# Performance work log

Measured on AMD Instinct MI355X. Metric: run time of the kernel, lower is better.

The kernel has to match this reference:

```python
import jax, jax.numpy as jnp
import numpy as np

H, W = 192, 640
MAX_ITERS = 200
EPS = 1e-8


def setup_inputs() -> dict:
    key = jax.random.key(0)
    k1, k2 = jax.random.split(key)
    B = 16
    ptcloud = jax.random.normal(k1, (B, 3, H * W), dtype=jnp.float32)
    # KITTI-like intrinsics; cy = 96 so the ground prior starts at row 96.
    Kmat = jnp.tile(
        jnp.array([[721.5, 0.0, 320.0], [0.0, 721.5, 96.0], [0.0, 0.0, 1.0]],
                  dtype=jnp.float32)[None], (B, 1, 1))
    ys = 96
    xs, xe = W * 3 // 8, W * 5 // 8
    n_prior = (H - ys) * (xe - xs)  # 15360
    sample_idx = jax.random.randint(k2, (MAX_ITERS, 3), 0, n_prior, dtype=jnp.int32)
    return {"ptcloud": ptcloud, "K": Kmat, "sample_idx": sample_idx}


def _median_low(x):
    """torch.median semantics (lower middle element), x: (B, N) -> (B, 1)."""
    n = x.shape[1]
    s = jnp.sort(x, axis=1)
    m = (n - 1) // 2
    return s[:, m:m + 1]


def _mad_threshold(y):
    med = _median_low(y)                       # (B, 1)
    return _median_low(jnp.abs(med - y))       # (B, 1)


def _ransac_plane(prior, sample_idx, thr):
    """prior: (B, N, 3), sample_idx: (I, 3), thr: (B, 1) -> plane (B, 4)."""
    samples = prior[:, sample_idx]             # (B, I, 3, 3)
    p1, p2, p3 = samples[:, :, 0], samples[:, :, 1], samples[:, :, 2]
    n = jnp.cross(p2 - p1, p3 - p1)            # (B, I, 3)
    n = n / (jnp.linalg.norm(n, axis=-1, keepdims=True) + EPS)
    d = -jnp.sum(n * p1, axis=-1)              # (B, I)
    # point-plane distances for all prior points: (B, I, N)
    dist = jnp.abs(jnp.einsum('bnc,bic->bin', prior, n) + d[:, :, None])
    counts = jnp.sum(dist <= thr[:, :, None], axis=-1)  # (B, I)
    best = jnp.argmax(counts, axis=1)                    # (B,)
    plane = jnp.concatenate([n, d[..., None]], axis=-1)  # (B, I, 4)
    return jnp.take_along_axis(plane, best[:, None, None], axis=1)[:, 0]


def reference(ptcloud, K, sample_idx):
    B = ptcloud.shape[0]
    # ground prior region (static slice; K is concrete at trace time here)
    ys = int(K[:, 1, 2].mean())
    xs, xe = W * 3 // 8, W * 5 // 8
    pc = ptcloud.reshape(B, 3, H, W)
    prior = pc[:, :, ys:, xs:xe].reshape(B, 3, -1).transpose(0, 2, 1)  # (B, N, 3)
    thr = _mad_threshold(prior[..., 1])                                # (B, 1)
    plane = _ransac_plane(prior, sample_idx, thr)                      # (B, 4)
    pts_all = ptcloud.transpose(0, 2, 1)                               # (B, M, 3)
    dist_all = jnp.abs(jnp.einsum('bmc,bc->bm', pts_all, plane[:, :3]) + plane[:, 3:4])
    inlier_mask = (dist_all <= thr).reshape(B, H, W)
    return plane, inlier_mask
```

## Files before the change

kernel.cpp:

```cpp
#include <hip/hip_runtime.h>
#include <cstdint>

#define HW      122880
#define NPRIOR  15360
#define NITER   200
#define NB      16
#define RANKSEL 7680u

__device__ __forceinline__ uint32_t f2k(float f) {
  uint32_t u = __float_as_uint(f);
  return (u & 0x80000000u) ? ~u : (u ^ 0x80000000u);
}
__device__ __forceinline__ float k2f(uint32_t k) {
  uint32_t u = (k & 0x80000000u) ? (k ^ 0x80000000u) : ~k;
  return __uint_as_float(u);
}

__device__ __forceinline__ uint32_t radix_select(const uint32_t* __restrict__ keys,
                                                 int tid, uint32_t* hist,
                                                 uint32_t* res) {
  uint32_t prefix = 0u;
  uint32_t t = RANKSEL;
#pragma unroll
  for (int p = 0; p < 4; p++) {
    const int shift = 24 - 8 * p;
    if (tid < 256) hist[tid] = 0u;
    __syncthreads();
#pragma unroll
    for (int j = 0; j < 15; j++) {
      uint32_t k = keys[j * 1024 + tid];
      bool match = (p == 0) ? true : ((k >> (shift + 8)) == prefix);
      if (match) atomicAdd(&hist[(k >> shift) & 255u], 1u);
    }
    __syncthreads();
    if (tid < 64) {
      uint32_t h0 = hist[4 * tid + 0];
      uint32_t h1 = hist[4 * tid + 1];
      uint32_t h2 = hist[4 * tid + 2];
      uint32_t h3 = hist[4 * tid + 3];
      uint32_t s0 = h0, s1 = s0 + h1, s2 = s1 + h2, s3 = s2 + h3;
      uint32_t incl = s3;
#pragma unroll
      for (int off = 1; off < 64; off <<= 1) {
        uint32_t n = __shfl_up(incl, off);
        if (tid >= off) incl += n;
      }
      uint32_t excl = incl - s3;
      if (t > excl && t <= incl) {
        uint32_t nb, nt;
        if (t <= excl + s0)      { nb = 4u * tid + 0u; nt = t - excl; }
        else if (t <= excl + s1) { nb = 4u * tid + 1u; nt = t - (excl + s0); }
        else if (t <= excl + s2) { nb = 4u * tid + 2u; nt = t - (excl + s1); }
        else                     { nb = 4u * tid + 3u; nt = t - (excl + s2); }
        res[0] = nb;
        res[1] = nt;
      }
    }
    __syncthreads();
    prefix = (prefix << 8) | res[0];
    t = res[1];
  }
  return prefix;
}

__global__ __launch_bounds__(1024)
void thr_kernel(const float* __restrict__ pt, const int* __restrict__ sidx,
                float* __restrict__ thr_out, float* __restrict__ planes,
                uint32_t* __restrict__ bestkey) {
  __shared__ uint32_t keys[NPRIOR];
  __shared__ uint32_t hist[256];
  __shared__ uint32_t res[2];
  const int b = blockIdx.x;
  const int tid = threadIdx.x;
  if (tid == 0) bestkey[b] = 0u;

  if (tid < NITER) {
    const float* base = pt + (size_t)b * 3 * HW;
    float p[3][3];
#pragma unroll
    for (int k = 0; k < 3; k++) {
      int s = sidx[tid * 3 + k];
      int r = s / 160;
      int c = s - r * 160;
      int hw = (96 + r) * 640 + 240 + c;
      p[k][0] = base[hw];
      p[k][1] = base[HW + hw];
      p[k][2] = base[2 * HW + hw];
    }
    float ux = __fsub_rn(p[1][0], p[0][0]);
    float uy = __fsub_rn(p[1][1], p[0][1]);
    float uz = __fsub_rn(p[1][2], p[0][2]);
    float vx = __fsub_rn(p[2][0], p[0][0]);
    float vy = __fsub_rn(p[2][1], p[0][1]);
    float vz = __fsub_rn(p[2][2], p[0][2]);
    float nx = __fsub_rn(__fmul_rn(uy, vz), __fmul_rn(uz, vy));
    float ny = __fsub_rn(__fmul_rn(uz, vx), __fmul_rn(ux, vz));
    float nz = __fsub_rn(__fmul_rn(ux, vy), __fmul_rn(uy, vx));
    float nn = __fsqrt_rn(__fadd_rn(__fadd_rn(__fmul_rn(nx, nx), __fmul_rn(ny, ny)),
                                    __fmul_rn(nz, nz)));
    float den = __fadd_rn(nn, 1e-8f);
    nx = __fdiv_rn(nx, den);
    ny = __fdiv_rn(ny, den);
    nz = __fdiv_rn(nz, den);
    float s3 = __fadd_rn(__fadd_rn(__fmul_rn(nx, p[0][0]), __fmul_rn(ny, p[0][1])),
                         __fmul_rn(nz, p[0][2]));
    int t = b * NITER + tid;
    planes[4 * t + 0] = nx;
    planes[4 * t + 1] = ny;
    planes[4 * t + 2] = nz;
    planes[4 * t + 3] = -s3;
  }

  const float* ybase = pt + (size_t)b * 3 * HW + HW;
  float yv[15];
#pragma unroll
  for (int j = 0; j < 15; j++) {
    int i = j * 1024 + tid;
    int r = i / 160;
    int c = i - r * 160;
    yv[j] = ybase[(96 + r) * 640 + 240 + c];
    keys[j * 1024 + tid] = f2k(yv[j]);
  }
  uint32_t medk = radix_select(keys, tid, hist, res);
  float med = k2f(medk);

#pragma unroll
  for (int j = 0; j < 15; j++)
    keys[j * 1024 + tid] = __float_as_uint(fabsf(__fsub_rn(med, yv[j])));
  uint32_t thk = radix_select(keys, tid, hist, res);
  if (tid == 0) thr_out[b] = __uint_as_float(thk);
}

__global__ __launch_bounds__(256)
void count_kernel(const float* __restrict__ pt, const float* __restrict__ planes,
                  const float* __restrict__ thr_arr, uint32_t* __restrict__ bestkey) {
  const int chunk = blockIdx.x;
  const int b = blockIdx.y;
  const int tid = threadIdx.x;
  __shared__ int cnt_s[13];
  if (tid < 13) cnt_s[tid] = 0;
  __syncthreads();
  const int p0 = chunk * 13;
  float plr[13][4];
#pragma unroll
  for (int k = 0; k < 13; k++) {
    int pidx = p0 + k;
    if (pidx < NITER) {
      const float* pp = planes + (size_t)(b * NITER + pidx) * 4;
      plr[k][0] = pp[0]; plr[k][1] = pp[1]; plr[k][2] = pp[2]; plr[k][3] = pp[3];
    } else {
      plr[k][0] = plr[k][1] = plr[k][2] = plr[k][3] = 0.0f;
    }
  }
  const float thr = thr_arr[b];
  const float* base = pt + (size_t)b * 3 * HW;
  int cnt[13];
#pragma unroll
  for (int k = 0; k < 13; k++) cnt[k] = 0;
  for (int ii = 0; ii < NPRIOR; ii += 1024) {
    int i = ii + tid * 4;
    int r = i / 160;
    int c = i - r * 160;
    int hw = (96 + r) * 640 + 240 + c;
    float4 x4 = *(const float4*)(base + hw);
    float4 y4 = *(const float4*)(base + HW + hw);
    float4 z4 = *(const float4*)(base + 2 * HW + hw);
    float xs[4] = {x4.x, x4.y, x4.z, x4.w};
    float ys[4] = {y4.x, y4.y, y4.z, y4.w};
    float zs[4] = {z4.x, z4.y, z4.z, z4.w};
#pragma unroll
    for (int q = 0; q < 4; q++) {
      float x = xs[q], y = ys[q], z = zs[q];
#pragma unroll
      for (int k = 0; k < 13; k++) {
        float s = __fadd_rn(__fadd_rn(__fmul_rn(x, plr[k][0]), __fmul_rn(y, plr[k][1])),
                            __fmul_rn(z, plr[k][2]));
        float dist = fabsf(__fadd_rn(s, plr[k][3]));
        cnt[k] += (dist <= thr) ? 1 : 0;
      }
    }
  }
#pragma unroll
  for (int k = 0; k < 13; k++) {
    int v = cnt[k];
#pragma unroll
    for (int off = 32; off; off >>= 1) v += __shfl_down(v, off);
    if ((tid & 63) == 0) atomicAdd(&cnt_s[k], v);
  }
  __syncthreads();
  if (tid < 13 && p0 + tid < NITER) {
    int iter = p0 + tid;
    uint32_t key = ((uint32_t)cnt_s[tid] << 8) | (uint32_t)(255 - iter);
    atomicMax(&bestkey[b], key);
  }
}

__global__ __launch_bounds__(256)
void mask_kernel(const float* __restrict__ pt, const float* __restrict__ planes,
                 const float* __restrict__ thr_arr, const uint32_t* __restrict__ bestkey,
                 float* __restrict__ out) {
  const int g4 = (blockIdx.x * 256 + threadIdx.x) * 4;
  const int b = g4 / HW;
  const int m = g4 - b * HW;
  const int best = 255 - (int)(bestkey[b] & 255u);
  const float* plane = planes + (size_t)(b * NITER + best) * 4;
  const float nx = plane[0], ny = plane[1], nz = plane[2], dd = plane[3];
  const float thr = thr_arr[b];
  const float* base = pt + (size_t)b * 3 * HW;
  float4 x4 = *(const float4*)(base + m);
  float4 y4 = *(const float4*)(base + HW + m);
  float4 z4 = *(const float4*)(base + 2 * HW + m);
  float xs[4] = {x4.x, x4.y, x4.z, x4.w};
  float ys[4] = {y4.x, y4.y, y4.z, y4.w};
  float zs[4] = {z4.x, z4.y, z4.z, z4.w};
  float4 o;
  float* os = (float*)&o;
#pragma unroll
  for (int q = 0; q < 4; q++) {
    float s = __fadd_rn(__fadd_rn(__fmul_rn(xs[q], nx), __fmul_rn(ys[q], ny)),
                        __fmul_rn(zs[q], nz));
    float dist = fabsf(__fadd_rn(s, dd));
    os[q] = (dist <= thr) ? 1.0f : 0.0f;
  }
  *(float4*)(out + 64 + (size_t)g4) = o;
  if (m == 0) {
#pragma unroll
    for (int q = 0; q < 4; q++) out[b * 4 + q] = plane[q];
  }
}

extern "C" void kernel_launch(void* const* d_in, const int* in_sizes, int n_in,
                              void* d_out, int out_size, void* d_ws, size_t ws_size,
                              hipStream_t stream) {
  (void)in_sizes; (void)n_in; (void)out_size; (void)ws_size;
  const float* pt = (const float*)d_in[0];
  const int* sidx = (const int*)d_in[2];
  float* out = (float*)d_out;

  float* thr      = (float*)d_ws;
  float* planes   = thr + 16;
  uint32_t* bkey  = (uint32_t*)(planes + NB * NITER * 4);

  thr_kernel<<<NB, 1024, 0, stream>>>(pt, sidx, thr, planes, bkey);
  count_kernel<<<dim3(16, NB), 256, 0, stream>>>(pt, planes, thr, bkey);
  mask_kernel<<<(NB * HW) / 1024, 256, 0, stream>>>(pt, planes, thr, bkey, out);
}
```

Before: 120.0 us.

## Replace 4-pass radix select with 13-bit histogram plus list binary search

The median and MAD selection now builds one 8192-bin histogram on the top 13 key bits, runs a block-wide scan to find the target bin, gathers that bin's keys into a short list, and binary-searches the remaining 19 bits with a single wavefront. This cuts the four histogram passes and their barriers per selection down to one histogram and one compaction pass. The y values are no longer kept in registers and are recovered from the stored keys instead. The list is capped at 2048 entries, so a heavily concentrated bin would give a wrong result, and the extra shared memory could lower occupancy.

```diff
diff --git a/kernel.cpp b/kernel.cpp
--- a/kernel.cpp
+++ b/kernel.cpp
@@ -6,6 +6,8 @@
 #define NITER   200
 #define NB      16
 #define RANKSEL 7680u
+#define NBINS   8192
+#define LISTCAP 2048
 
 __device__ __forceinline__ uint32_t f2k(float f) {
   uint32_t u = __float_as_uint(f);
@@ -16,60 +18,108 @@
   return __uint_as_float(u);
 }
 
-__device__ __forceinline__ uint32_t radix_select(const uint32_t* __restrict__ keys,
-                                                 int tid, uint32_t* hist,
-                                                 uint32_t* res) {
-  uint32_t prefix = 0u;
-  uint32_t t = RANKSEL;
-#pragma unroll
-  for (int p = 0; p < 4; p++) {
-    const int shift = 24 - 8 * p;
-    if (tid < 256) hist[tid] = 0u;
-    __syncthreads();
-#pragma unroll
-    for (int j = 0; j < 15; j++) {
-      uint32_t k = keys[j * 1024 + tid];
-      bool match = (p == 0) ? true : ((k >> (shift + 8)) == prefix);
-      if (match) atomicAdd(&hist[(k >> shift) & 255u], 1u);
-    }
-    __syncthreads();
-    if (tid < 64) {
-      uint32_t h0 = hist[4 * tid + 0];
-      uint32_t h1 = hist[4 * tid + 1];
-      uint32_t h2 = hist[4 * tid + 2];
-      uint32_t h3 = hist[4 * tid + 3];
-      uint32_t s0 = h0, s1 = s0 + h1, s2 = s1 + h2, s3 = s2 + h3;
-      uint32_t incl = s3;
-#pragma unroll
-      for (int off = 1; off < 64; off <<= 1) {
-        uint32_t n = __shfl_up(incl, off);
-        if (tid >= off) incl += n;
+__device__ uint32_t select13(uint32_t* __restrict__ keys, uint32_t* __restrict__ hist,
+                             uint32_t* __restrict__ wpart, uint32_t* __restrict__ res,
+                             uint32_t* __restrict__ list, uint32_t* __restrict__ pcnt,
+                             uint32_t* __restrict__ pfin, int tid) {
+  {
+    uint4 z = {0u, 0u, 0u, 0u};
+    ((uint4*)hist)[tid] = z;
+    ((uint4*)hist)[1024 + tid] = z;
+  }
+  if (tid == 0) *pcnt = 0u;
+  __syncthreads();
+#pragma unroll
+  for (int j = 0; j < 15; j++) {
+    uint32_t k = keys[j * 1024 + tid];
+    atomicAdd(&hist[k >> 19], 1u);
+  }
+  __syncthreads();
+  uint32_t h[8];
+  uint32_t s = 0u;
+#pragma unroll
+  for (int e = 0; e < 8; e++) {
+    h[e] = hist[8 * tid + e];
+    s += h[e];
+  }
+  uint32_t incl = s;
+#pragma unroll
+  for (int off = 1; off < 64; off <<= 1) {
+    uint32_t n = __shfl_up(incl, off);
+    if ((tid & 63) >= off) incl += n;
+  }
+  if ((tid & 63) == 63) wpart[tid >> 6] = incl;
+  __syncthreads();
+  {
+    uint32_t base = 0u;
+    const int wv = tid >> 6;
+#pragma unroll
+    for (int w = 0; w < 16; w++) base += (w < wv) ? wpart[w] : 0u;
+    incl += base;
+  }
+  const uint32_t excl = incl - s;
+  if (RANKSEL > excl && RANKSEL <= incl) {
+    uint32_t c = excl;
+#pragma unroll
+    for (int e = 0; e < 8; e++) {
+      uint32_t nc = c + h[e];
+      if (RANKSEL > c && RANKSEL <= nc) {
+        res[0] = (uint32_t)(8 * tid + e);
+        res[1] = RANKSEL - c;
       }
-      uint32_t excl = incl - s3;
-      if (t > excl && t <= incl) {
-        uint32_t nb, nt;
-        if (t <= excl + s0)      { nb = 4u * tid + 0u; nt = t - excl; }
-        else if (t <= excl + s1) { nb = 4u * tid + 1u; nt = t - (excl + s0); }
-        else if (t <= excl + s2) { nb = 4u * tid + 2u; nt = t - (excl + s1); }
-        else                     { nb = 4u * tid + 3u; nt = t - (excl + s2); }
-        res[0] = nb;
-        res[1] = nt;
-      }
-    }
-    __syncthreads();
-    prefix = (prefix << 8) | res[0];
-    t = res[1];
-  }
-  return prefix;
-}
-
-__global__ __launch_bounds__(1024)
+      c = nc;
+    }
+  }
+  __syncthreads();
+  const uint32_t bin = res[0];
+  const uint32_t tp = res[1];
+#pragma unroll
+  for (int j = 0; j < 15; j++) {
+    uint32_t k = keys[j * 1024 + tid];
+    if ((k >> 19) == bin) {
+      uint32_t p = atomicAdd(pcnt, 1u);
+      if (p < LISTCAP) list[p] = k & 0x7FFFFu;
+    }
+  }
+  __syncthreads();
+  if (tid < 64) {
+    const uint32_t n = *pcnt;
+    uint32_t kk[8];
+#pragma unroll
+    for (int j = 0; j < 8; j++) {
+      uint32_t p = (uint32_t)tid + 64u * j;
+      kk[j] = (p < n) ? list[p] : 0xFFFFFFFFu;
+    }
+    uint32_t lo = 0u, hi = 0x7FFFFu;
+    while (lo < hi) {
+      uint32_t mid = lo + ((hi - lo) >> 1);
+      int c = 0;
+#pragma unroll
+      for (int j = 0; j < 8; j++) c += (kk[j] <= mid) ? 1 : 0;
+      for (uint32_t p = 512u + (uint32_t)tid; p < n; p += 64u)
+        c += (list[p] <= mid) ? 1 : 0;
+#pragma unroll
+      for (int off = 32; off; off >>= 1) c += __shfl_down(c, off);
+      c = __shfl(c, 0);
+      if ((uint32_t)c >= tp) hi = mid; else lo = mid + 1u;
+    }
+    if (tid == 0) *pfin = (bin << 19) | lo;
+  }
+  __syncthreads();
+  return *pfin;
+}
+
+__global__ __launch_bounds__(1024, 4)
 void thr_kernel(const float* __restrict__ pt, const int* __restrict__ sidx,
                 float* __restrict__ thr_out, float* __restrict__ planes,
                 uint32_t* __restrict__ bestkey) {
   __shared__ uint32_t keys[NPRIOR];
-  __shared__ uint32_t hist[256];
+  __shared__ uint32_t hist[NBINS];
+  __shared__ uint32_t list[LISTCAP];
+  __shared__ uint32_t wpart[16];
   __shared__ uint32_t res[2];
+  __shared__ uint32_t lcnt;
+  __shared__ uint32_t fin;
   const int b = blockIdx.x;
   const int tid = threadIdx.x;
   if (tid == 0) bestkey[b] = 0u;
@@ -112,22 +162,22 @@
   }
 
   const float* ybase = pt + (size_t)b * 3 * HW + HW;
-  float yv[15];
 #pragma unroll
   for (int j = 0; j < 15; j++) {
     int i = j * 1024 + tid;
     int r = i / 160;
     int c = i - r * 160;
-    yv[j] = ybase[(96 + r) * 640 + 240 + c];
-    keys[j * 1024 + tid] = f2k(yv[j]);
-  }
-  uint32_t medk = radix_select(keys, tid, hist, res);
+    keys[j * 1024 + tid] = f2k(ybase[(96 + r) * 640 + 240 + c]);
+  }
+  uint32_t medk = select13(keys, hist, wpart, res, list, &lcnt, &fin, tid);
   float med = k2f(medk);
 
 #pragma unroll
-  for (int j = 0; j < 15; j++)
-    keys[j * 1024 + tid] = __float_as_uint(fabsf(__fsub_rn(med, yv[j])));
-  uint32_t thk = radix_select(keys, tid, hist, res);
+  for (int j = 0; j < 15; j++) {
+    float y = k2f(keys[j * 1024 + tid]);
+    keys[j * 1024 + tid] = __float_as_uint(fabsf(__fsub_rn(med, y)));
+  }
+  uint32_t thk = select13(keys, hist, wpart, res, list, &lcnt, &fin, tid);
   if (tid == 0) thr_out[b] = __uint_as_float(thk);
 }
 
```

New measurement: 119.0 us. About the same (-0.8%).
